# Kernel optimization log

Measured on AMD Instinct MI355X. Metric: run time of the kernel, lower is better.

The kernel has to match this reference:

```python
import jax, jax.numpy as jnp
import numpy as np

B, N, D = 4, 4096, 1024
H, M = 16, 256
DH = D // H

def setup_inputs() -> dict:
    key = jax.random.key(0)
    ks = jax.random.split(key, 6)
    x = jax.random.normal(ks[0], (B, N, D), dtype=jnp.float32)
    Wqkv = jax.random.normal(ks[1], (D, 3 * D), dtype=jnp.float32) * 0.02
    bqkv = jnp.zeros((3 * D,), dtype=jnp.float32)
    Wout = jax.random.normal(ks[2], (D, D), dtype=jnp.float32) * 0.02
    bout = jnp.zeros((D,), dtype=jnp.float32)
    omega = jax.random.normal(ks[3], (DH, M), dtype=jnp.float32)
    return {"x": x, "Wqkv": Wqkv, "bqkv": bqkv, "Wout": Wout, "bout": bout, "omega": omega}

def _feature_map(t, omega):
    # phi(t) = exp(t @ omega - ||t||^2 / 2); t: [b,h,n,dh] -> [b,h,n,m]
    t_omega = jnp.einsum('bhnd,dm->bhnm', t, omega)
    norm_sq = 0.5 * jnp.sum(t * t, axis=-1, keepdims=True)
    return jnp.exp(t_omega - norm_sq)

def reference(x, Wqkv, bqkv, Wout, bout, omega):
    b, n, d = x.shape
    qkv = x @ Wqkv + bqkv                      # [b,n,3d]
    q, k, v = jnp.split(qkv, 3, axis=-1)
    def to_heads(t):
        return t.reshape(b, n, H, DH).transpose(0, 2, 1, 3)  # [b,h,n,dh]
    q, k, v = to_heads(q), to_heads(k), to_heads(v)
    q_prime = _feature_map(q, omega)           # [b,h,n,m]
    k_prime = _feature_map(k, omega)           # [b,h,n,m]
    k_sum = jnp.sum(k_prime, axis=2)           # [b,h,m]
    denominator = jnp.einsum('bhnm,bhm->bhn', q_prime, k_sum)[..., None]  # [b,h,n,1]
    k_v = jnp.einsum('bhnm,bhnd->bhmd', k_prime, v)                       # [b,h,m,dh]
    numerator = jnp.einsum('bhnm,bhmd->bhnd', q_prime, k_v)               # [b,h,n,dh]
    out = numerator / (denominator + 1e-6)
    out = out.transpose(0, 2, 1, 3).reshape(b, n, d)
    return out @ Wout + bout
```

## Files before the change

### kernel.cpp

```cpp
#include <hip/hip_runtime.h>
#include <hip/hip_bf16.h>

#define B_SZ 4
#define N_SZ 4096
#define D_SZ 1024
#define H_SZ 16
#define M_SZ 256
#define DH_SZ 64
#define ROWS (B_SZ * N_SZ)
#define KSPLIT 4
#define QROWS 64
#define KV_TOT (64 * M_SZ * DH_SZ)
#define KS_TOT (64 * M_SZ)

typedef unsigned short u16;
typedef __attribute__((ext_vector_type(8))) short bf16x8;
typedef __attribute__((ext_vector_type(4))) short s16x4;
typedef __attribute__((ext_vector_type(4))) float f32x4;

static __device__ inline u16 f2bf(float f) {
    __hip_bfloat16 h = __float2bfloat16(f);
    return *reinterpret_cast<u16*>(&h);
}
static __device__ inline float bf2f(u16 u) {
    return __bfloat162float(*reinterpret_cast<__hip_bfloat16*>(&u));
}

static __device__ inline void gl_lds16(const void* g, void* l) {
    void* gg = const_cast<void*>(g);
    __builtin_amdgcn_global_load_lds(
        (__attribute__((address_space(1))) void*)gg,
        (__attribute__((address_space(3))) void*)l, 16, 0, 0);
}

__global__ __launch_bounds__(256) void cvt_f32_bf16(
    const float* __restrict__ src, u16* __restrict__ dst)
{
    const long i = ((long)blockIdx.x * 256 + threadIdx.x) * 8;
    float4 v0 = *(const float4*)(src + i);
    float4 v1 = *(const float4*)(src + i + 4);
    union { u16 s[8]; bf16x8 v; } o;
    o.s[0] = f2bf(v0.x); o.s[1] = f2bf(v0.y); o.s[2] = f2bf(v0.z); o.s[3] = f2bf(v0.w);
    o.s[4] = f2bf(v1.x); o.s[5] = f2bf(v1.y); o.s[6] = f2bf(v1.z); o.s[7] = f2bf(v1.w);
    *(bf16x8*)(dst + i) = o.v;
}

__global__ __launch_bounds__(256) void transpose_cvt(
    const float* __restrict__ src, u16* __restrict__ dst, int R, int C)
{
    __shared__ float tile[32][33];
    const int c0 = blockIdx.x * 32, r0 = blockIdx.y * 32;
    const int tx = threadIdx.x & 31, ty = threadIdx.x >> 5;
    #pragma unroll
    for (int p = 0; p < 4; ++p)
        tile[ty + 8 * p][tx] = src[(long)(r0 + ty + 8 * p) * C + c0 + tx];
    __syncthreads();
    #pragma unroll
    for (int p = 0; p < 4; ++p)
        dst[(long)(c0 + ty + 8 * p) * R + r0 + tx] = f2bf(tile[tx][ty + 8 * p]);
}

template <typename OUT>
__global__ __launch_bounds__(256) void gemm_mfma_bt(
    const u16* __restrict__ A, const u16* __restrict__ Bt,
    const float* __restrict__ bias, OUT* __restrict__ C,
    int Nc, int K)
{
    __shared__ u16 As[128 * 32];
    __shared__ u16 Bs[128 * 32];
    const int t = threadIdx.x;
    const int w = t >> 6, l = t & 63;
    const int wr = w >> 1, wc = w & 1;
    const long brow = (long)blockIdx.y * 128;
    const long bcol = (long)blockIdx.x * 128;

    const int sr = l >> 2;
    const int sc = (l & 3) * 8;
    const u16* aS0 = A + (brow + w * 16 + sr) * (long)K + sc;
    const u16* aS1 = A + (brow + 64 + w * 16 + sr) * (long)K + sc;
    const u16* bS0 = Bt + (bcol + w * 16 + sr) * (long)K + sc;
    const u16* bS1 = Bt + (bcol + 64 + w * 16 + sr) * (long)K + sc;
    u16* aD0 = As + (w) * 512;
    u16* aD1 = As + (w + 4) * 512;
    u16* bD0 = Bs + (w) * 512;
    u16* bD1 = Bs + (w + 4) * 512;

    f32x4 acc[4][4];
    #pragma unroll
    for (int m = 0; m < 4; ++m)
        #pragma unroll
        for (int n = 0; n < 4; ++n)
            acc[m][n] = (f32x4){0.f, 0.f, 0.f, 0.f};

    const int fr = l & 15;
    const int fk = (l >> 4) * 8;

    for (int k0 = 0; k0 < K; k0 += 32) {
        __syncthreads();
        gl_lds16(aS0 + k0, aD0);
        gl_lds16(aS1 + k0, aD1);
        gl_lds16(bS0 + k0, bD0);
        gl_lds16(bS1 + k0, bD1);
        __syncthreads();
        bf16x8 af[4], bfv[4];
        #pragma unroll
        for (int m = 0; m < 4; ++m)
            af[m] = *(const bf16x8*)(As + (wr * 64 + m * 16 + fr) * 32 + fk);
        #pragma unroll
        for (int n = 0; n < 4; ++n)
            bfv[n] = *(const bf16x8*)(Bs + (wc * 64 + n * 16 + fr) * 32 + fk);
        #pragma unroll
        for (int m = 0; m < 4; ++m)
            #pragma unroll
            for (int n = 0; n < 4; ++n)
                acc[m][n] = __builtin_amdgcn_mfma_f32_16x16x32_bf16(
                    af[m], bfv[n], acc[m][n], 0, 0, 0);
    }

    const int fq = l >> 4;
    float bv[4];
    #pragma unroll
    for (int n = 0; n < 4; ++n)
        bv[n] = bias[bcol + wc * 64 + n * 16 + fr];
    #pragma unroll
    for (int m = 0; m < 4; ++m) {
        #pragma unroll
        for (int n = 0; n < 4; ++n) {
            const long col = bcol + wc * 64 + n * 16 + fr;
            #pragma unroll
            for (int r = 0; r < 4; ++r) {
                const long row = brow + wr * 64 + m * 16 + fq * 4 + r;
                const float v = acc[m][n][r] + bv[n];
                if constexpr (sizeof(OUT) == 2)
                    ((u16*)C)[row * Nc + col] = f2bf(v);
                else
                    ((float*)C)[row * Nc + col] = v;
            }
        }
    }
}

__global__ __launch_bounds__(256) void kfeat(
    const u16* __restrict__ qkv, const u16* __restrict__ omT,
    float* __restrict__ kvpart, float* __restrict__ kspart)
{
    __shared__ u16 omTs[2][256][32];
    __shared__ u16 kTs[2][256][32];
    __shared__ u16 vTs[2][80][32];
    __shared__ u16 kcs[2][64][32];
    __shared__ float norms[64];

    const int t = threadIdx.x;
    const int w = t >> 6, l = t & 63, fr = l & 15, fq = l >> 4;
    const int blk = blockIdx.x;
    const int s = blk & (KSPLIT - 1);
    const int bh = blk / KSPLIT;
    const int b = bh >> 4, h = bh & 15;
    const long rowbase = (long)b * N_SZ + s * (N_SZ / KSPLIT);

    for (int i = t; i < 2048; i += 256) {
        const int m = i >> 3, d0 = (i & 7) * 8;
        *(bf16x8*)&omTs[d0 >> 5][m][d0 & 31] = *(const bf16x8*)(omT + m * 64 + d0);
    }
    for (int i = t; i < 2 * 16 * 32; i += 256) {
        const int kc = i >> 9, rr = (i >> 5) & 15, j = i & 31;
        vTs[kc][64 + rr][j] = (rr == 0) ? (u16)0x3F80 : (u16)0;
    }

    f32x4 acc2[4][5];
    #pragma unroll
    for (int mi = 0; mi < 4; ++mi)
        #pragma unroll
        for (int dt = 0; dt < 5; ++dt)
            acc2[mi][dt] = (f32x4){0.f, 0.f, 0.f, 0.f};

    for (int c = 0; c < (N_SZ / KSPLIT) / 64; ++c) {
        const long r0 = rowbase + c * 64;
        for (int i = t; i < 512; i += 256) {
            const int n = i >> 3, d0 = (i & 7) * 8;
            *(bf16x8*)&kcs[d0 >> 5][n][d0 & 31] =
                *(const bf16x8*)(qkv + (r0 + n) * 3072 + D_SZ + h * 64 + d0);
            union { bf16x8 v; u16 s[8]; } uv;
            uv.v = *(const bf16x8*)(qkv + (r0 + n) * 3072 + 2 * D_SZ + h * 64 + d0);
            #pragma unroll
            for (int j = 0; j < 8; ++j) vTs[n >> 5][d0 + j][n & 31] = uv.s[j];
        }
        {
            const int r = t >> 2, p = t & 3;
            float ss = 0.f;
            const u16* krow = qkv + (r0 + r) * 3072 + D_SZ + h * 64 + p * 16;
            #pragma unroll
            for (int j = 0; j < 16; ++j) { const float v = bf2f(krow[j]); ss += v * v; }
            ss += __shfl_xor(ss, 1, 64);
            ss += __shfl_xor(ss, 2, 64);
            if (p == 0) norms[r] = 0.5f * ss;
        }
        __syncthreads();
        f32x4 acc1[16];
        #pragma unroll
        for (int mt = 0; mt < 16; ++mt) acc1[mt] = (f32x4){0.f, 0.f, 0.f, 0.f};
        #pragma unroll
        for (int kc = 0; kc < 2; ++kc) {
            bf16x8 bfr = *(const bf16x8*)&kcs[kc][w * 16 + fr][fq * 8];
            #pragma unroll
            for (int mt = 0; mt < 16; ++mt) {
                bf16x8 afr = *(const bf16x8*)&omTs[kc][mt * 16 + fr][fq * 8];
                acc1[mt] = __builtin_amdgcn_mfma_f32_16x16x32_bf16(afr, bfr, acc1[mt], 0, 0, 0);
            }
        }
        const float nrm = norms[w * 16 + fr];
        #pragma unroll
        for (int mt = 0; mt < 16; ++mt) {
            #pragma unroll
            for (int r = 0; r < 4; ++r) {
                const float e = __expf(acc1[mt][r] - nrm);
                kTs[w >> 1][mt * 16 + fq * 4 + r][(w & 1) * 16 + fr] = f2bf(e);
            }
        }
        __syncthreads();
        #pragma unroll
        for (int kc = 0; kc < 2; ++kc) {
            bf16x8 bfv[5];
            #pragma unroll
            for (int dt = 0; dt < 5; ++dt)
                bfv[dt] = *(const bf16x8*)&vTs[kc][dt * 16 + fr][fq * 8];
            #pragma unroll
            for (int mi = 0; mi < 4; ++mi) {
                bf16x8 afr = *(const bf16x8*)&kTs[kc][w * 64 + mi * 16 + fr][fq * 8];
                #pragma unroll
                for (int dt = 0; dt < 5; ++dt)
                    acc2[mi][dt] = __builtin_amdgcn_mfma_f32_16x16x32_bf16(
                        afr, bfv[dt], acc2[mi][dt], 0, 0, 0);
            }
        }
        __syncthreads();
    }

    float* kvp = kvpart + (long)blk * 16384;
    #pragma unroll
    for (int mi = 0; mi < 4; ++mi) {
        #pragma unroll
        for (int dt = 0; dt < 4; ++dt)
            #pragma unroll
            for (int r = 0; r < 4; ++r)
                kvp[(w * 64 + mi * 16 + fq * 4 + r) * 64 + dt * 16 + fr] = acc2[mi][dt][r];
        if (fr == 0) {
            #pragma unroll
            for (int r = 0; r < 4; ++r)
                kspart[blk * 256 + w * 64 + mi * 16 + fq * 4 + r] = acc2[mi][4][r];
        }
    }
}

__global__ __launch_bounds__(256) void reduce2(
    const float* __restrict__ kvpart, const float* __restrict__ kspart,
    u16* __restrict__ kvT, float* __restrict__ ksfin)
{
    const int i = blockIdx.x * 256 + threadIdx.x;
    if (i < KV_TOT) {
        const int bh = i >> 14, d = (i >> 8) & 63, m = i & 255;
        float s = 0.f;
        #pragma unroll
        for (int p = 0; p < KSPLIT; ++p)
            s += kvpart[(long)(bh * KSPLIT + p) * 16384 + m * 64 + d];
        kvT[i] = f2bf(s);
    } else if (i < KV_TOT + KS_TOT) {
        const int j = i - KV_TOT, bh = j >> 8, m = j & 255;
        float s = 0.f;
        #pragma unroll
        for (int p = 0; p < KSPLIT; ++p)
            s += kspart[(bh * KSPLIT + p) * 256 + m];
        ksfin[j] = s;
    }
}

__global__ __launch_bounds__(256) void qfeat(
    const u16* __restrict__ qkv, const u16* __restrict__ omT,
    const u16* __restrict__ kvT, const float* __restrict__ ksfin,
    u16* __restrict__ att)
{
    __shared__ u16 shA[16384];
    __shared__ u16 qps[8][64][32];
    __shared__ u16 qcs[2][64][32];
    __shared__ float ksum[256];
    __shared__ float norms[64];
    __shared__ float den[64];

    const int t = threadIdx.x;
    const int w = t >> 6, l = t & 63, fr = l & 15, fq = l >> 4;
    const int blk = blockIdx.x;
    const int c = blk & 63;
    const int bh = blk >> 6;
    const int b = bh >> 4, h = bh & 15;
    const long r0 = (long)b * N_SZ + c * QROWS;

    for (int i = t; i < 2048; i += 256) {
        const int m = i >> 3, d0 = (i & 7) * 8;
        *(bf16x8*)&shA[(d0 >> 5) * 8192 + m * 32 + (d0 & 31)] =
            *(const bf16x8*)(omT + m * 64 + d0);
    }
    for (int i = t; i < 512; i += 256) {
        const int n = i >> 3, d0 = (i & 7) * 8;
        *(bf16x8*)&qcs[d0 >> 5][n][d0 & 31] =
            *(const bf16x8*)(qkv + (r0 + n) * 3072 + h * 64 + d0);
    }
    ksum[t] = ksfin[bh * 256 + t];
    {
        const int r = t >> 2, p = t & 3;
        float ss = 0.f;
        const u16* qrow = qkv + (r0 + r) * 3072 + h * 64 + p * 16;
        #pragma unroll
        for (int j = 0; j < 16; ++j) { const float v = bf2f(qrow[j]); ss += v * v; }
        ss += __shfl_xor(ss, 1, 64);
        ss += __shfl_xor(ss, 2, 64);
        if (p == 0) norms[r] = 0.5f * ss;
    }
    __syncthreads();

    f32x4 acc1[16];
    #pragma unroll
    for (int mt = 0; mt < 16; ++mt) acc1[mt] = (f32x4){0.f, 0.f, 0.f, 0.f};
    #pragma unroll
    for (int kc = 0; kc < 2; ++kc) {
        bf16x8 bfr = *(const bf16x8*)&qcs[kc][w * 16 + fr][fq * 8];
        #pragma unroll
        for (int mt = 0; mt < 16; ++mt) {
            bf16x8 afr = *(const bf16x8*)&shA[kc * 8192 + (mt * 16 + fr) * 32 + fq * 8];
            acc1[mt] = __builtin_amdgcn_mfma_f32_16x16x32_bf16(afr, bfr, acc1[mt], 0, 0, 0);
        }
    }
    const float nrm = norms[w * 16 + fr];
    float denp = 0.f;
    #pragma unroll
    for (int mt = 0; mt < 16; ++mt) {
        union { s16x4 v; u16 s[4]; } pk;
        #pragma unroll
        for (int r = 0; r < 4; ++r) {
            const float e = __expf(acc1[mt][r] - nrm);
            denp += e * ksum[mt * 16 + fq * 4 + r];
            pk.s[r] = f2bf(e);
        }
        *(s16x4*)&qps[mt >> 1][w * 16 + fr][(mt & 1) * 16 + fq * 4] = pk.v;
    }
    __syncthreads();

    const u16* kvb = kvT + bh * 16384;
    for (int i = t; i < 2048; i += 256) {
        const int d = i >> 5, m0 = (i & 31) * 8;
        *(bf16x8*)&shA[(m0 >> 5) * 2048 + d * 32 + (m0 & 31)] =
            *(const bf16x8*)(kvb + d * 256 + m0);
    }
    denp += __shfl_xor(denp, 16, 64);
    denp += __shfl_xor(denp, 32, 64);
    if (l < 16) den[w * 16 + fr] = denp;
    __syncthreads();

    f32x4 acc3[4];
    #pragma unroll
    for (int dt = 0; dt < 4; ++dt) acc3[dt] = (f32x4){0.f, 0.f, 0.f, 0.f};
    #pragma unroll
    for (int kc = 0; kc < 8; ++kc) {
        bf16x8 afr = *(const bf16x8*)&qps[kc][w * 16 + fr][fq * 8];
        #pragma unroll
        for (int dt = 0; dt < 4; ++dt) {
            bf16x8 bfr = *(const bf16x8*)&shA[kc * 2048 + (dt * 16 + fr) * 32 + fq * 8];
            acc3[dt] = __builtin_amdgcn_mfma_f32_16x16x32_bf16(afr, bfr, acc3[dt], 0, 0, 0);
        }
    }
    #pragma unroll
    for (int r = 0; r < 4; ++r) {
        const int n = w * 16 + fq * 4 + r;
        const float dn = den[n] + 1e-6f;
        #pragma unroll
        for (int dt = 0; dt < 4; ++dt)
            att[(r0 + n) * 1024 + h * 64 + dt * 16 + fr] = f2bf(acc3[dt][r] / dn);
    }
}

extern "C" void kernel_launch(void* const* d_in, const int* in_sizes, int n_in,
                              void* d_out, int out_size, void* d_ws, size_t ws_size,
                              hipStream_t stream)
{
    const float* x     = (const float*)d_in[0];
    const float* Wqkv  = (const float*)d_in[1];
    const float* bqkv  = (const float*)d_in[2];
    const float* Wout  = (const float*)d_in[3];
    const float* bout  = (const float*)d_in[4];
    const float* omega = (const float*)d_in[5];
    float* out = (float*)d_out;

    char* wp = (char*)d_ws;
    u16*   xb     = (u16*)wp;
    float* kvpart = (float*)wp;
    float* kspart = (float*)(wp + 16777216);
    u16*   att    = (u16*)wp;
    u16*   qkv    = (u16*)(wp + 34078720);
    u16*   Wqkv_t = (u16*)(wp + 134742016);
    u16*   kvT    = (u16*)(wp + 134742016);
    float* ksfin  = (float*)(wp + 134742016 + 2097152);
    u16*   Wout_t = (u16*)(wp + 141033472);
    u16*   omT    = (u16*)(wp + 143130624);

    cvt_f32_bf16<<<ROWS * D_SZ / (256 * 8), 256, 0, stream>>>(x, xb);
    {
        dim3 g(3 * D_SZ / 32, D_SZ / 32);
        transpose_cvt<<<g, 256, 0, stream>>>(Wqkv, Wqkv_t, D_SZ, 3 * D_SZ);
    }
    {
        dim3 g(D_SZ / 32, D_SZ / 32);
        transpose_cvt<<<g, 256, 0, stream>>>(Wout, Wout_t, D_SZ, D_SZ);
    }
    {
        dim3 g(M_SZ / 32, DH_SZ / 32);
        transpose_cvt<<<g, 256, 0, stream>>>(omega, omT, DH_SZ, M_SZ);
    }
    {
        dim3 g(3 * D_SZ / 128, ROWS / 128);
        gemm_mfma_bt<u16><<<g, 256, 0, stream>>>(xb, Wqkv_t, bqkv, qkv, 3 * D_SZ, D_SZ);
    }
    kfeat<<<64 * KSPLIT, 256, 0, stream>>>(qkv, omT, kvpart, kspart);
    {
        int total = KV_TOT + KS_TOT;
        reduce2<<<(total + 255) / 256, 256, 0, stream>>>(kvpart, kspart, kvT, ksfin);
    }
    qfeat<<<64 * 64, 256, 0, stream>>>(qkv, omT, kvT, ksfin, att);
    {
        dim3 g(D_SZ / 128, ROWS / 128);
        gemm_mfma_bt<float><<<g, 256, 0, stream>>>(att, Wout_t, bout, out, D_SZ, D_SZ);
    }
}
```

Measured before the change: 475.4 us.

## Widen feature kernels to 512 threads with register-prefetched row chunks

kfeat and qfeat now run 512-thread blocks that handle 128-row chunks, loading the next chunk's K/V or Q rows into registers while the current chunk is on the MFMA units. qfeat becomes persistent over 512 rows per (batch, head), so omega and the kv matrix are staged into LDS once per block instead of once per 64 rows. Row norms are computed from the prefetched registers rather than re-read from global memory. This aims to hide global load latency and remove redundant LDS staging, at the cost of fewer blocks (512 in qfeat), more LDS per block and extra barriers per chunk.

```diff
diff --git a/kernel.cpp b/kernel.cpp
--- a/kernel.cpp
+++ b/kernel.cpp
@@ -9,7 +9,6 @@
 #define DH_SZ 64
 #define ROWS (B_SZ * N_SZ)
 #define KSPLIT 4
-#define QROWS 64
 #define KV_TOT (64 * M_SZ * DH_SZ)
 #define KS_TOT (64 * M_SZ)
 
@@ -140,93 +139,105 @@
     }
 }
 
-__global__ __launch_bounds__(256) void kfeat(
+__global__ __launch_bounds__(512) void kfeat(
     const u16* __restrict__ qkv, const u16* __restrict__ omT,
     float* __restrict__ kvpart, float* __restrict__ kspart)
 {
     __shared__ u16 omTs[2][256][32];
-    __shared__ u16 kTs[2][256][32];
-    __shared__ u16 vTs[2][80][32];
-    __shared__ u16 kcs[2][64][32];
-    __shared__ float norms[64];
+    __shared__ u16 kTbuf[32768];
+    __shared__ u16 vTs[4][80][32];
+    __shared__ float norms[128];
 
     const int t = threadIdx.x;
     const int w = t >> 6, l = t & 63, fr = l & 15, fq = l >> 4;
     const int blk = blockIdx.x;
-    const int s = blk & (KSPLIT - 1);
-    const int bh = blk / KSPLIT;
+    const int s = blk & (KSPLIT - 1), bh = blk >> 2;
     const int b = bh >> 4, h = bh & 15;
     const long rowbase = (long)b * N_SZ + s * (N_SZ / KSPLIT);
 
-    for (int i = t; i < 2048; i += 256) {
+    const int pn = t >> 2, pd = (t & 3) * 16;
+    const u16* kp = qkv + (rowbase + pn) * 3072 + D_SZ + h * 64 + pd;
+    const u16* vp = qkv + (rowbase + pn) * 3072 + 2 * D_SZ + h * 64 + pd;
+    bf16x8 pk0 = *(const bf16x8*)kp, pk1 = *(const bf16x8*)(kp + 8);
+    bf16x8 pv0 = *(const bf16x8*)vp, pv1 = *(const bf16x8*)(vp + 8);
+
+    for (int i = t; i < 2048; i += 512) {
         const int m = i >> 3, d0 = (i & 7) * 8;
         *(bf16x8*)&omTs[d0 >> 5][m][d0 & 31] = *(const bf16x8*)(omT + m * 64 + d0);
     }
-    for (int i = t; i < 2 * 16 * 32; i += 256) {
+    for (int i = t; i < 2048; i += 512) {
         const int kc = i >> 9, rr = (i >> 5) & 15, j = i & 31;
         vTs[kc][64 + rr][j] = (rr == 0) ? (u16)0x3F80 : (u16)0;
     }
 
-    f32x4 acc2[4][5];
-    #pragma unroll
-    for (int mi = 0; mi < 4; ++mi)
+    f32x4 acc2[2][5];
+    #pragma unroll
+    for (int mi = 0; mi < 2; ++mi)
         #pragma unroll
         for (int dt = 0; dt < 5; ++dt)
             acc2[mi][dt] = (f32x4){0.f, 0.f, 0.f, 0.f};
 
-    for (int c = 0; c < (N_SZ / KSPLIT) / 64; ++c) {
-        const long r0 = rowbase + c * 64;
-        for (int i = t; i < 512; i += 256) {
-            const int n = i >> 3, d0 = (i & 7) * 8;
-            *(bf16x8*)&kcs[d0 >> 5][n][d0 & 31] =
-                *(const bf16x8*)(qkv + (r0 + n) * 3072 + D_SZ + h * 64 + d0);
-            union { bf16x8 v; u16 s[8]; } uv;
-            uv.v = *(const bf16x8*)(qkv + (r0 + n) * 3072 + 2 * D_SZ + h * 64 + d0);
-            #pragma unroll
-            for (int j = 0; j < 8; ++j) vTs[n >> 5][d0 + j][n & 31] = uv.s[j];
-        }
-        {
-            const int r = t >> 2, p = t & 3;
-            float ss = 0.f;
-            const u16* krow = qkv + (r0 + r) * 3072 + D_SZ + h * 64 + p * 16;
-            #pragma unroll
-            for (int j = 0; j < 16; ++j) { const float v = bf2f(krow[j]); ss += v * v; }
-            ss += __shfl_xor(ss, 1, 64);
-            ss += __shfl_xor(ss, 2, 64);
-            if (p == 0) norms[r] = 0.5f * ss;
-        }
-        __syncthreads();
+    u16* kcs = kTbuf + 24576;
+
+    for (int c = 0; c < 8; ++c) {
+        *(bf16x8*)(kcs + (pd >> 5) * 4096 + pn * 32 + (pd & 31)) = pk0;
+        *(bf16x8*)(kcs + (pd >> 5) * 4096 + pn * 32 + (pd & 31) + 8) = pk1;
+        union { bf16x8 v; u16 u[8]; } uk0, uk1, uv0, uv1;
+        uk0.v = pk0; uk1.v = pk1; uv0.v = pv0; uv1.v = pv1;
+        #pragma unroll
+        for (int j = 0; j < 8; ++j) {
+            vTs[pn >> 5][pd + j][pn & 31] = uv0.u[j];
+            vTs[pn >> 5][pd + 8 + j][pn & 31] = uv1.u[j];
+        }
+        float ss = 0.f;
+        #pragma unroll
+        for (int j = 0; j < 8; ++j) {
+            float a = bf2f(uk0.u[j]), bb = bf2f(uk1.u[j]);
+            ss += a * a + bb * bb;
+        }
+        ss += __shfl_xor(ss, 1, 64);
+        ss += __shfl_xor(ss, 2, 64);
+        if ((t & 3) == 0) norms[pn] = 0.5f * ss;
+        __syncthreads();
+        if (c < 7) {
+            const long off = (long)(c + 1) * 128 * 3072;
+            pk0 = *(const bf16x8*)(kp + off);
+            pk1 = *(const bf16x8*)(kp + off + 8);
+            pv0 = *(const bf16x8*)(vp + off);
+            pv1 = *(const bf16x8*)(vp + off + 8);
+        }
         f32x4 acc1[16];
         #pragma unroll
         for (int mt = 0; mt < 16; ++mt) acc1[mt] = (f32x4){0.f, 0.f, 0.f, 0.f};
         #pragma unroll
         for (int kc = 0; kc < 2; ++kc) {
-            bf16x8 bfr = *(const bf16x8*)&kcs[kc][w * 16 + fr][fq * 8];
+            bf16x8 bfr = *(const bf16x8*)(kcs + kc * 4096 + (w * 16 + fr) * 32 + fq * 8);
             #pragma unroll
             for (int mt = 0; mt < 16; ++mt) {
                 bf16x8 afr = *(const bf16x8*)&omTs[kc][mt * 16 + fr][fq * 8];
                 acc1[mt] = __builtin_amdgcn_mfma_f32_16x16x32_bf16(afr, bfr, acc1[mt], 0, 0, 0);
             }
         }
+        __syncthreads();
         const float nrm = norms[w * 16 + fr];
         #pragma unroll
         for (int mt = 0; mt < 16; ++mt) {
             #pragma unroll
             for (int r = 0; r < 4; ++r) {
                 const float e = __expf(acc1[mt][r] - nrm);
-                kTs[w >> 1][mt * 16 + fq * 4 + r][(w & 1) * 16 + fr] = f2bf(e);
-            }
-        }
-        __syncthreads();
-        #pragma unroll
-        for (int kc = 0; kc < 2; ++kc) {
+                kTbuf[(w >> 1) * 8192 + (mt * 16 + fq * 4 + r) * 32 + (w & 1) * 16 + fr] = f2bf(e);
+            }
+        }
+        __syncthreads();
+        #pragma unroll
+        for (int kc = 0; kc < 4; ++kc) {
             bf16x8 bfv[5];
             #pragma unroll
             for (int dt = 0; dt < 5; ++dt)
                 bfv[dt] = *(const bf16x8*)&vTs[kc][dt * 16 + fr][fq * 8];
             #pragma unroll
-            for (int mi = 0; mi < 4; ++mi) {
-                bf16x8 afr = *(const bf16x8*)&kTs[kc][w * 64 + mi * 16 + fr][fq * 8];
+            for (int mi = 0; mi < 2; ++mi) {
+                bf16x8 afr = *(const bf16x8*)(kTbuf + kc * 8192 + ((w * 2 + mi) * 16 + fr) * 32 + fq * 8);
                 #pragma unroll
                 for (int dt = 0; dt < 5; ++dt)
                     acc2[mi][dt] = __builtin_amdgcn_mfma_f32_16x16x32_bf16(
@@ -238,16 +249,17 @@
 
     float* kvp = kvpart + (long)blk * 16384;
     #pragma unroll
-    for (int mi = 0; mi < 4; ++mi) {
+    for (int mi = 0; mi < 2; ++mi) {
+        const int m0 = (w * 2 + mi) * 16 + fq * 4;
         #pragma unroll
         for (int dt = 0; dt < 4; ++dt)
             #pragma unroll
             for (int r = 0; r < 4; ++r)
-                kvp[(w * 64 + mi * 16 + fq * 4 + r) * 64 + dt * 16 + fr] = acc2[mi][dt][r];
+                kvp[(m0 + r) * 64 + dt * 16 + fr] = acc2[mi][dt][r];
         if (fr == 0) {
             #pragma unroll
             for (int r = 0; r < 4; ++r)
-                kspart[blk * 256 + w * 64 + mi * 16 + fq * 4 + r] = acc2[mi][4][r];
+                kspart[blk * 256 + m0 + r] = acc2[mi][4][r];
         }
     }
 }
@@ -274,106 +286,114 @@
     }
 }
 
-__global__ __launch_bounds__(256) void qfeat(
+__global__ __launch_bounds__(512) void qfeat(
     const u16* __restrict__ qkv, const u16* __restrict__ omT,
     const u16* __restrict__ kvT, const float* __restrict__ ksfin,
     u16* __restrict__ att)
 {
-    __shared__ u16 shA[16384];
-    __shared__ u16 qps[8][64][32];
-    __shared__ u16 qcs[2][64][32];
+    __shared__ u16 omTs[2][256][32];
+    __shared__ u16 kvTs[8][64][32];
+    __shared__ u16 qbuf[32768];
     __shared__ float ksum[256];
-    __shared__ float norms[64];
-    __shared__ float den[64];
+    __shared__ float norms[128];
+    __shared__ float den[128];
 
     const int t = threadIdx.x;
     const int w = t >> 6, l = t & 63, fr = l & 15, fq = l >> 4;
     const int blk = blockIdx.x;
-    const int c = blk & 63;
-    const int bh = blk >> 6;
+    const int slice = blk & 7, bh = blk >> 3;
     const int b = bh >> 4, h = bh & 15;
-    const long r0 = (long)b * N_SZ + c * QROWS;
-
-    for (int i = t; i < 2048; i += 256) {
+    const long rowbase = (long)b * N_SZ + slice * 512;
+
+    const int pn = t >> 2, pd = (t & 3) * 16;
+    const u16* qp = qkv + (rowbase + pn) * 3072 + h * 64 + pd;
+    bf16x8 pq0 = *(const bf16x8*)qp, pq1 = *(const bf16x8*)(qp + 8);
+
+    for (int i = t; i < 2048; i += 512) {
         const int m = i >> 3, d0 = (i & 7) * 8;
-        *(bf16x8*)&shA[(d0 >> 5) * 8192 + m * 32 + (d0 & 31)] =
-            *(const bf16x8*)(omT + m * 64 + d0);
-    }
-    for (int i = t; i < 512; i += 256) {
-        const int n = i >> 3, d0 = (i & 7) * 8;
-        *(bf16x8*)&qcs[d0 >> 5][n][d0 & 31] =
-            *(const bf16x8*)(qkv + (r0 + n) * 3072 + h * 64 + d0);
-    }
-    ksum[t] = ksfin[bh * 256 + t];
-    {
-        const int r = t >> 2, p = t & 3;
+        *(bf16x8*)&omTs[d0 >> 5][m][d0 & 31] = *(const bf16x8*)(omT + m * 64 + d0);
+    }
+    const u16* kvb = kvT + bh * 16384;
+    for (int i = t; i < 2048; i += 512) {
+        const int d = i >> 5, m0 = (i & 31) * 8;
+        *(bf16x8*)&kvTs[m0 >> 5][d][m0 & 31] = *(const bf16x8*)(kvb + d * 256 + m0);
+    }
+    if (t < 256) ksum[t] = ksfin[bh * 256 + t];
+
+    u16* qcs = qbuf + 24576;
+
+    for (int c = 0; c < 4; ++c) {
+        *(bf16x8*)(qcs + (pd >> 5) * 4096 + pn * 32 + (pd & 31)) = pq0;
+        *(bf16x8*)(qcs + (pd >> 5) * 4096 + pn * 32 + (pd & 31) + 8) = pq1;
+        union { bf16x8 v; u16 u[8]; } uq0, uq1;
+        uq0.v = pq0; uq1.v = pq1;
         float ss = 0.f;
-        const u16* qrow = qkv + (r0 + r) * 3072 + h * 64 + p * 16;
-        #pragma unroll
-        for (int j = 0; j < 16; ++j) { const float v = bf2f(qrow[j]); ss += v * v; }
+        #pragma unroll
+        for (int j = 0; j < 8; ++j) {
+            float a = bf2f(uq0.u[j]), bb = bf2f(uq1.u[j]);
+            ss += a * a + bb * bb;
+        }
         ss += __shfl_xor(ss, 1, 64);
         ss += __shfl_xor(ss, 2, 64);
-        if (p == 0) norms[r] = 0.5f * ss;
-    }
-    __syncthreads();
-
-    f32x4 acc1[16];
-    #pragma unroll
-    for (int mt = 0; mt < 16; ++mt) acc1[mt] = (f32x4){0.f, 0.f, 0.f, 0.f};
-    #pragma unroll
-    for (int kc = 0; kc < 2; ++kc) {
-        bf16x8 bfr = *(const bf16x8*)&qcs[kc][w * 16 + fr][fq * 8];
+        if ((t & 3) == 0) norms[pn] = 0.5f * ss;
+        __syncthreads();
+        if (c < 3) {
+            const long off = (long)(c + 1) * 128 * 3072;
+            pq0 = *(const bf16x8*)(qp + off);
+            pq1 = *(const bf16x8*)(qp + off + 8);
+        }
+        f32x4 acc1[16];
+        #pragma unroll
+        for (int mt = 0; mt < 16; ++mt) acc1[mt] = (f32x4){0.f, 0.f, 0.f, 0.f};
+        #pragma unroll
+        for (int kc = 0; kc < 2; ++kc) {
+            bf16x8 bfr = *(const bf16x8*)(qcs + kc * 4096 + (w * 16 + fr) * 32 + fq * 8);
+            #pragma unroll
+            for (int mt = 0; mt < 16; ++mt) {
+                bf16x8 afr = *(const bf16x8*)&omTs[kc][mt * 16 + fr][fq * 8];
+                acc1[mt] = __builtin_amdgcn_mfma_f32_16x16x32_bf16(afr, bfr, acc1[mt], 0, 0, 0);
+            }
+        }
+        __syncthreads();
+        const float nrm = norms[w * 16 + fr];
+        float denp = 0.f;
         #pragma unroll
         for (int mt = 0; mt < 16; ++mt) {
-            bf16x8 afr = *(const bf16x8*)&shA[kc * 8192 + (mt * 16 + fr) * 32 + fq * 8];
-            acc1[mt] = __builtin_amdgcn_mfma_f32_16x16x32_bf16(afr, bfr, acc1[mt], 0, 0, 0);
-        }
-    }
-    const float nrm = norms[w * 16 + fr];
-    float denp = 0.f;
-    #pragma unroll
-    for (int mt = 0; mt < 16; ++mt) {
-        union { s16x4 v; u16 s[4]; } pk;
+            union { s16x4 v; u16 u[4]; } pk;
+            #pragma unroll
+            for (int r = 0; r < 4; ++r) {
+                const float e = __expf(acc1[mt][r] - nrm);
+                denp += e * ksum[mt * 16 + fq * 4 + r];
+                pk.u[r] = f2bf(e);
+            }
+            *(s16x4*)(qbuf + (mt >> 1) * 4096 + (w * 16 + fr) * 32 + (mt & 1) * 16 + fq * 4) = pk.v;
+        }
+        denp += __shfl_xor(denp, 16, 64);
+        denp += __shfl_xor(denp, 32, 64);
+        if (l < 16) den[w * 16 + fr] = denp;
+        __syncthreads();
+        f32x4 acc3[4];
+        #pragma unroll
+        for (int dt = 0; dt < 4; ++dt) acc3[dt] = (f32x4){0.f, 0.f, 0.f, 0.f};
+        #pragma unroll
+        for (int kc = 0; kc < 8; ++kc) {
+            bf16x8 afr = *(const bf16x8*)(qbuf + kc * 4096 + (w * 16 + fr) * 32 + fq * 8);
+            #pragma unroll
+            for (int dt = 0; dt < 4; ++dt) {
+                bf16x8 bfr = *(const bf16x8*)&kvTs[kc][dt * 16 + fr][fq * 8];
+                acc3[dt] = __builtin_amdgcn_mfma_f32_16x16x32_bf16(afr, bfr, acc3[dt], 0, 0, 0);
+            }
+        }
         #pragma unroll
         for (int r = 0; r < 4; ++r) {
-            const float e = __expf(acc1[mt][r] - nrm);
-            denp += e * ksum[mt * 16 + fq * 4 + r];
-            pk.s[r] = f2bf(e);
-        }
-        *(s16x4*)&qps[mt >> 1][w * 16 + fr][(mt & 1) * 16 + fq * 4] = pk.v;
-    }
-    __syncthreads();
-
-    const u16* kvb = kvT + bh * 16384;
-    for (int i = t; i < 2048; i += 256) {
-        const int d = i >> 5, m0 = (i & 31) * 8;
-        *(bf16x8*)&shA[(m0 >> 5) * 2048 + d * 32 + (m0 & 31)] =
-            *(const bf16x8*)(kvb + d * 256 + m0);
-    }
-    denp += __shfl_xor(denp, 16, 64);
-    denp += __shfl_xor(denp, 32, 64);
-    if (l < 16) den[w * 16 + fr] = denp;
-    __syncthreads();
-
-    f32x4 acc3[4];
-    #pragma unroll
-    for (int dt = 0; dt < 4; ++dt) acc3[dt] = (f32x4){0.f, 0.f, 0.f, 0.f};
-    #pragma unroll
-    for (int kc = 0; kc < 8; ++kc) {
-        bf16x8 afr = *(const bf16x8*)&qps[kc][w * 16 + fr][fq * 8];
-        #pragma unroll
-        for (int dt = 0; dt < 4; ++dt) {
-            bf16x8 bfr = *(const bf16x8*)&shA[kc * 2048 + (dt * 16 + fr) * 32 + fq * 8];
-            acc3[dt] = __builtin_amdgcn_mfma_f32_16x16x32_bf16(afr, bfr, acc3[dt], 0, 0, 0);
-        }
-    }
-    #pragma unroll
-    for (int r = 0; r < 4; ++r) {
-        const int n = w * 16 + fq * 4 + r;
-        const float dn = den[n] + 1e-6f;
-        #pragma unroll
-        for (int dt = 0; dt < 4; ++dt)
-            att[(r0 + n) * 1024 + h * 64 + dt * 16 + fr] = f2bf(acc3[dt][r] / dn);
+            const int n = w * 16 + fq * 4 + r;
+            const float dn = den[n] + 1e-6f;
+            #pragma unroll
+            for (int dt = 0; dt < 4; ++dt)
+                att[(rowbase + c * 128 + n) * 1024 + h * 64 + dt * 16 + fr] =
+                    f2bf(acc3[dt][r] / dn);
+        }
+        __syncthreads();
     }
 }
 
@@ -418,12 +438,12 @@
         dim3 g(3 * D_SZ / 128, ROWS / 128);
         gemm_mfma_bt<u16><<<g, 256, 0, stream>>>(xb, Wqkv_t, bqkv, qkv, 3 * D_SZ, D_SZ);
     }
-    kfeat<<<64 * KSPLIT, 256, 0, stream>>>(qkv, omT, kvpart, kspart);
+    kfeat<<<64 * KSPLIT, 512, 0, stream>>>(qkv, omT, kvpart, kspart);
     {
         int total = KV_TOT + KS_TOT;
         reduce2<<<(total + 255) / 256, 256, 0, stream>>>(kvpart, kspart, kvT, ksfin);
     }
-    qfeat<<<64 * 64, 256, 0, stream>>>(qkv, omT, kvT, ksfin, att);
+    qfeat<<<64 * 8, 512, 0, stream>>>(qkv, omT, kvT, ksfin, att);
     {
         dim3 g(D_SZ / 128, ROWS / 128);
         gemm_mfma_bt<float><<<g, 256, 0, stream>>>(att, Wout_t, bout, out, D_SZ, D_SZ);
```

After: 456.6 us. 1.04x faster.
